# Performance work log

Measured on AMD Instinct MI355X. Metric: run time of the kernel, lower is better.

Reference implementation:

```python
import jax, jax.numpy as jnp
import numpy as np

N_NODES = 50000


def _sage_conv(x, src, dst, W_l, b_l, W_r):
    # PyG SAGEConv (aggr='mean'): out = lin_l(mean_{j in N(i)} x_j) + lin_r(x_i)
    # lin_l has bias, lin_r has no bias.
    neigh_sum = jax.ops.segment_sum(x[src], dst, num_segments=N_NODES)  # [N, F]
    deg = jax.ops.segment_sum(jnp.ones_like(dst, dtype=x.dtype), dst, num_segments=N_NODES)
    neigh_mean = neigh_sum / jnp.maximum(deg, 1.0)[:, None]
    return neigh_mean @ W_l.T + b_l + x @ W_r.T


def setup_inputs() -> dict:
    key = jax.random.key(0)
    ks = jax.random.split(key, 8)
    D, H, C = 768, 128, 4
    x = jax.random.normal(ks[0], (N_NODES, D), dtype=jnp.float32)
    edge_index = jax.random.randint(ks[1], (2, 800000), 0, N_NODES, dtype=jnp.int64)
    s1 = 1.0 / np.sqrt(D)
    s2 = 1.0 / np.sqrt(H)
    return {
        "x": x,
        "edge_index": edge_index,
        "W1_l": jax.random.uniform(ks[2], (H, D), jnp.float32, -s1, s1),
        "b1_l": jnp.zeros((H,), jnp.float32),
        "W1_r": jax.random.uniform(ks[3], (H, D), jnp.float32, -s1, s1),
        "W2_l": jax.random.uniform(ks[4], (C, H), jnp.float32, -s2, s2),
        "b2_l": jnp.zeros((C,), jnp.float32),
        "W2_r": jax.random.uniform(ks[5], (C, H), jnp.float32, -s2, s2),
    }


def reference(x, edge_index, W1_l, b1_l, W1_r, W2_l, b2_l, W2_r):
    src, dst = edge_index[0], edge_index[1]
    h = jax.nn.relu(_sage_conv(x, src, dst, W1_l, b1_l, W1_r))  # [N, H]
    out = _sage_conv(h, src, dst, W2_l, b2_l, W2_r)  # [N, C]
    return out
```

## Files before the change

kernel.cpp:

```cpp
#include <hip/hip_runtime.h>


typedef __bf16 bf16x8 __attribute__((ext_vector_type(8)));
typedef float  f32x4  __attribute__((ext_vector_type(4)));

__device__ __forceinline__ float bf16_lo(uint32_t w) {
    union { uint32_t u; float f; } c; c.u = w << 16; return c.f;
}
__device__ __forceinline__ float bf16_hi(uint32_t w) {
    union { uint32_t u; float f; } c; c.u = w & 0xffff0000u; return c.f;
}

__global__ __launch_bounds__(256)
void prep(const float* __restrict__ W1l, const float* __restrict__ W1r,
          __bf16* __restrict__ Wb, int* __restrict__ deg, int N)
{
    int i = blockIdx.x * 256 + threadIdx.x;
    if (i < N) deg[i] = 0;
    if (i < 256 * 768) {
        int n = i / 768, k = i - n * 768;
        float v = (n < 128) ? W1l[n * 768 + k] : W1r[(n - 128) * 768 + k];
        Wb[i] = (__bf16)v;
    }
}

__global__ __launch_bounds__(256)
void csr_count(const int* __restrict__ ei, int* __restrict__ deg, int E)
{
    int e = blockIdx.x * 256 + threadIdx.x;
    if (e >= E) return;
    atomicAdd(&deg[ei[E + e]], 1);
}

__global__ __launch_bounds__(1024)
void scan1(const int* __restrict__ deg, int* __restrict__ row_ptr,
           int* __restrict__ partials, int N)
{
    __shared__ int buf[1024];
    int i = blockIdx.x * 1024 + threadIdx.x;
    int v = (i < N) ? deg[i] : 0;
    int val = v;
    buf[threadIdx.x] = val;
    __syncthreads();
    for (int off = 1; off < 1024; off <<= 1) {
        int t = (threadIdx.x >= (unsigned)off) ? buf[threadIdx.x - off] : 0;
        __syncthreads();
        val += t;
        buf[threadIdx.x] = val;
        __syncthreads();
    }
    if (i < N) row_ptr[i] = val - v;
    if (threadIdx.x == 1023) partials[blockIdx.x] = val;
}

__global__ __launch_bounds__(1024)
void scan23(int* __restrict__ row_ptr, int* __restrict__ cursor,
            const int* __restrict__ partials, int N, int E, int nb)
{
    __shared__ int soff;
    int b = blockIdx.x;
    if (threadIdx.x < 64) {
        int lane = threadIdx.x;
        int v = (lane < nb) ? partials[lane] : 0;
        int s = v;
        #pragma unroll
        for (int off = 1; off < 64; off <<= 1) {
            int t = __shfl_up(s, off);
            if (lane >= off) s += t;
        }
        if (lane == b) soff = s - v;
    }
    __syncthreads();
    int off = soff;
    int i = b * 1024 + threadIdx.x;
    if (i < N) {
        int v = row_ptr[i] + off;
        row_ptr[i] = v;
        cursor[i]  = v;
    }
    if (b == 0 && threadIdx.x == 0) row_ptr[N] = E;
}

__global__ __launch_bounds__(256)
void gemm_fill(const float* __restrict__ A, const __bf16* __restrict__ Bw,
               __bf16* __restrict__ Cb, int M, int gblocks,
               const int* __restrict__ ei, int* __restrict__ cursor,
               int* __restrict__ csr_src, int E)
{
    constexpr int LDK = 72;
    __shared__ __bf16 As[64][LDK];
    __shared__ __bf16 Bs[64][LDK];
    const int tid = threadIdx.x;

    if ((int)blockIdx.x >= gblocks) {
        int e = (blockIdx.x - gblocks) * 256 + tid;
        if (e < E) {
            int src = ei[e];
            int dst = ei[E + e];
            int pos = atomicAdd(&cursor[dst], 1);
            csr_src[pos] = src;
        }
        return;
    }

    const int p   = blockIdx.x;
    const int xcd = p & 7, kk = p >> 3;
    const int q   = gblocks >> 3, rem = gblocks & 7;
    const int base = (xcd < rem) ? xcd * (q + 1) : rem * (q + 1) + (xcd - rem) * q;
    const int job = base + kk;
    const int bm  = (job >> 2) * 64;
    const int bn  = (job & 3) * 64;

    const int lane = tid & 63;
    const int wave = tid >> 6;
    const int wr = wave >> 1, wc = wave & 1;
    const int l15 = lane & 15;
    const int lk  = lane >> 4;

    f32x4 acc[2][2] = {};
    float4 apref[2][2];
    bf16x8 bpref[2];

    auto load_tile = [&](int k0) {
        #pragma unroll
        for (int it = 0; it < 2; ++it) {
            int v = it * 256 + tid;
            int row = v >> 3, kc = (v & 7) << 3;
            if (bm + row < M) {
                const float* src = A + (size_t)(bm + row) * 768 + k0 + kc;
                apref[it][0] = *(const float4*)src;
                apref[it][1] = *(const float4*)(src + 4);
            } else {
                apref[it][0] = make_float4(0.f, 0.f, 0.f, 0.f);
                apref[it][1] = make_float4(0.f, 0.f, 0.f, 0.f);
            }
            bpref[it] = *(const bf16x8*)(Bw + (size_t)(bn + row) * 768 + k0 + kc);
        }
    };

    load_tile(0);
    for (int kt = 0; kt < 12; ++kt) {
        if (kt) __syncthreads();
        #pragma unroll
        for (int it = 0; it < 2; ++it) {
            int v = it * 256 + tid;
            int row = v >> 3, kc = (v & 7) << 3;
            float4 f0 = apref[it][0], f1 = apref[it][1];
            bf16x8 b;
            b[0] = (__bf16)f0.x; b[1] = (__bf16)f0.y;
            b[2] = (__bf16)f0.z; b[3] = (__bf16)f0.w;
            b[4] = (__bf16)f1.x; b[5] = (__bf16)f1.y;
            b[6] = (__bf16)f1.z; b[7] = (__bf16)f1.w;
            *(bf16x8*)&As[row][kc] = b;
            *(bf16x8*)&Bs[row][kc] = bpref[it];
        }
        __syncthreads();
        if (kt < 11) load_tile((kt + 1) * 64);

        #pragma unroll
        for (int ks = 0; ks < 2; ++ks) {
            int koff = ks * 32 + lk * 8;
            bf16x8 af[2], bfr[2];
            #pragma unroll
            for (int i = 0; i < 2; ++i)
                af[i] = *(const bf16x8*)&As[wr * 32 + i * 16 + l15][koff];
            #pragma unroll
            for (int j = 0; j < 2; ++j)
                bfr[j] = *(const bf16x8*)&Bs[wc * 32 + j * 16 + l15][koff];
            #pragma unroll
            for (int i = 0; i < 2; ++i)
                #pragma unroll
                for (int j = 0; j < 2; ++j)
                    acc[i][j] = __builtin_amdgcn_mfma_f32_16x16x32_bf16(
                        af[i], bfr[j], acc[i][j], 0, 0, 0);
        }
    }

    __syncthreads();
    #pragma unroll
    for (int i = 0; i < 2; ++i)
        #pragma unroll
        for (int j = 0; j < 2; ++j)
            #pragma unroll
            for (int v = 0; v < 4; ++v)
                As[wr * 32 + i * 16 + lk * 4 + v][wc * 32 + j * 16 + l15] =
                    (__bf16)acc[i][j][v];
    __syncthreads();
    #pragma unroll
    for (int it = 0; it < 2; ++it) {
        int idx = it * 256 + tid;
        int row = idx >> 3, ch = idx & 7;
        if (bm + row < M)
            *(bf16x8*)(Cb + (size_t)(bm + row) * 256 + bn + ch * 8) =
                *(const bf16x8*)&As[row][ch * 8];
    }
}

__global__ __launch_bounds__(256)
void sage1_fused(const int* __restrict__ row_ptr, const int* __restrict__ csr_src,
                 const __bf16* __restrict__ pq, const float* __restrict__ b1,
                 const float* __restrict__ W2l, const float* __restrict__ W2r,
                 float* __restrict__ r, float* __restrict__ s, int N)
{
    __shared__ float Wl[512], Wr[512];
    for (int i = threadIdx.x; i < 512; i += 256) {
        Wl[i] = W2l[i];
        Wr[i] = W2r[i];
    }
    __syncthreads();

    int wid  = threadIdx.x >> 6;
    int lane = threadIdx.x & 63;
    int g = lane >> 3;
    int l = lane & 7;
    int n = blockIdx.x * 4 + wid;
    if (n >= N) return;
    int beg = row_ptr[n], end = row_ptr[n + 1];

    float a0[8] = {}, a1[8] = {};
    for (int eb = beg; eb < end; eb += 64) {
        int cnt = min(64, end - eb);
        int id = (eb + lane < end) ? csr_src[eb + lane] : 0;
        for (int t = 0; t < cnt; t += 8) {
            int src = __shfl(id, t + g);
            if (t + g < cnt) {
                const __bf16* row = pq + (size_t)src * 256;
                uint4 w0 = *(const uint4*)(row + l * 8);
                uint4 w1 = *(const uint4*)(row + 64 + l * 8);
                a0[0] += bf16_lo(w0.x); a0[1] += bf16_hi(w0.x);
                a0[2] += bf16_lo(w0.y); a0[3] += bf16_hi(w0.y);
                a0[4] += bf16_lo(w0.z); a0[5] += bf16_hi(w0.z);
                a0[6] += bf16_lo(w0.w); a0[7] += bf16_hi(w0.w);
                a1[0] += bf16_lo(w1.x); a1[1] += bf16_hi(w1.x);
                a1[2] += bf16_lo(w1.y); a1[3] += bf16_hi(w1.y);
                a1[4] += bf16_lo(w1.z); a1[5] += bf16_hi(w1.z);
                a1[6] += bf16_lo(w1.w); a1[7] += bf16_hi(w1.w);
            }
        }
    }
    #pragma unroll
    for (int c = 0; c < 8; ++c) {
        a0[c] += __shfl_xor(a0[c], 8);  a1[c] += __shfl_xor(a1[c], 8);
        a0[c] += __shfl_xor(a0[c], 16); a1[c] += __shfl_xor(a1[c], 16);
        a0[c] += __shfl_xor(a0[c], 32); a1[c] += __shfl_xor(a1[c], 32);
    }

    float inv = 1.0f / fmaxf((float)(end - beg), 1.0f);
    const __bf16* qrow = pq + (size_t)n * 256 + 128;
    uint4  qw0 = *(const uint4*)(qrow + l * 8);
    uint4  qw1 = *(const uint4*)(qrow + 64 + l * 8);
    float4 bv00 = *(const float4*)(b1 + l * 8);
    float4 bv01 = *(const float4*)(b1 + l * 8 + 4);
    float4 bv10 = *(const float4*)(b1 + 64 + l * 8);
    float4 bv11 = *(const float4*)(b1 + 64 + l * 8 + 4);
    float h0[8], h1[8];
    h0[0] = fmaxf(a0[0] * inv + bv00.x + bf16_lo(qw0.x), 0.f);
    h0[1] = fmaxf(a0[1] * inv + bv00.y + bf16_hi(qw0.x), 0.f);
    h0[2] = fmaxf(a0[2] * inv + bv00.z + bf16_lo(qw0.y), 0.f);
    h0[3] = fmaxf(a0[3] * inv + bv00.w + bf16_hi(qw0.y), 0.f);
    h0[4] = fmaxf(a0[4] * inv + bv01.x + bf16_lo(qw0.z), 0.f);
    h0[5] = fmaxf(a0[5] * inv + bv01.y + bf16_hi(qw0.z), 0.f);
    h0[6] = fmaxf(a0[6] * inv + bv01.z + bf16_lo(qw0.w), 0.f);
    h0[7] = fmaxf(a0[7] * inv + bv01.w + bf16_hi(qw0.w), 0.f);
    h1[0] = fmaxf(a1[0] * inv + bv10.x + bf16_lo(qw1.x), 0.f);
    h1[1] = fmaxf(a1[1] * inv + bv10.y + bf16_hi(qw1.x), 0.f);
    h1[2] = fmaxf(a1[2] * inv + bv10.z + bf16_lo(qw1.y), 0.f);
    h1[3] = fmaxf(a1[3] * inv + bv10.w + bf16_hi(qw1.y), 0.f);
    h1[4] = fmaxf(a1[4] * inv + bv11.x + bf16_lo(qw1.z), 0.f);
    h1[5] = fmaxf(a1[5] * inv + bv11.y + bf16_hi(qw1.z), 0.f);
    h1[6] = fmaxf(a1[6] * inv + bv11.z + bf16_lo(qw1.w), 0.f);
    h1[7] = fmaxf(a1[7] * inv + bv11.w + bf16_hi(qw1.w), 0.f);

    float part[8];
    #pragma unroll
    for (int c = 0; c < 4; ++c) {
        float pl = 0.f, pr = 0.f;
        #pragma unroll
        for (int j = 0; j < 8; ++j) {
            pl = fmaf(h0[j], Wl[c * 128 + l * 8 + j], pl);
            pl = fmaf(h1[j], Wl[c * 128 + 64 + l * 8 + j], pl);
            pr = fmaf(h0[j], Wr[c * 128 + l * 8 + j], pr);
            pr = fmaf(h1[j], Wr[c * 128 + 64 + l * 8 + j], pr);
        }
        part[c] = pl; part[4 + c] = pr;
    }
    #pragma unroll
    for (int off = 4; off; off >>= 1)
        #pragma unroll
        for (int c = 0; c < 8; ++c)
            part[c] += __shfl_xor(part[c], off);
    if (lane == 0) {
        *(float4*)(r + (size_t)n * 4) = make_float4(part[0], part[1], part[2], part[3]);
        *(float4*)(s + (size_t)n * 4) = make_float4(part[4], part[5], part[6], part[7]);
    }
}

__global__ __launch_bounds__(256)
void sage2_gather(const int* __restrict__ row_ptr, const int* __restrict__ csr_src,
                  const float* __restrict__ r, const float* __restrict__ s,
                  const float* __restrict__ b2, float* __restrict__ out, int N)
{
    int t = blockIdx.x * 256 + threadIdx.x;
    if (t >= N * 4) return;
    int n = t >> 2, c = t & 3;
    int beg = row_ptr[n], end = row_ptr[n + 1];
    float acc = 0.f;
    for (int e = beg; e < end; ++e)
        acc += r[(size_t)csr_src[e] * 4 + c];
    out[t] = acc / fmaxf((float)(end - beg), 1.0f) + b2[c] + s[t];
}

extern "C" void kernel_launch(void* const* d_in, const int* in_sizes, int n_in,
                              void* d_out, int out_size, void* d_ws, size_t ws_size,
                              hipStream_t stream)
{
    const float* x   = (const float*)d_in[0];
    const int*   ei  = (const int*)d_in[1];
    const float* W1l = (const float*)d_in[2];
    const float* b1l = (const float*)d_in[3];
    const float* W1r = (const float*)d_in[4];
    const float* W2l = (const float*)d_in[5];
    const float* b2l = (const float*)d_in[6];
    const float* W2r = (const float*)d_in[7];
    float* out = (float*)d_out;

    const int N = in_sizes[0] / 768;
    const int E = in_sizes[1] / 2;
    const int NB = (N + 1023) / 1024;
    const int mtiles  = (N + 63) / 64;
    const int gblocks = mtiles * 4;
    const int fblocks = (E + 255) / 256;

    char* ws = (char*)d_ws;
    size_t off = 0;
    auto alloc = [&](size_t bytes) -> void* {
        void* pp = ws + off;
        off += (bytes + 255) & ~(size_t)255;
        return pp;
    };
    __bf16* pq      = (__bf16*)alloc((size_t)N * 256 * 2);
    float*  r       = (float*)alloc((size_t)N * 4 * 4);
    float*  s       = (float*)alloc((size_t)N * 4 * 4);
    __bf16* Wb      = (__bf16*)alloc((size_t)256 * 768 * 2);
    int*    deg     = (int*)alloc((size_t)N * 4);
    int*    row_ptr = (int*)alloc((size_t)(N + 1) * 4);
    int*    cursor  = (int*)alloc((size_t)N * 4);
    int*    csr_src = (int*)alloc((size_t)E * 4);
    int*    partials= (int*)alloc((size_t)64 * 4);

    prep<<<(256 * 768 + 255) / 256, 256, 0, stream>>>(W1l, W1r, Wb, deg, N);

    csr_count<<<(E + 255) / 256, 256, 0, stream>>>(ei, deg, E);
    scan1<<<NB, 1024, 0, stream>>>(deg, row_ptr, partials, N);
    scan23<<<NB, 1024, 0, stream>>>(row_ptr, cursor, partials, N, E, NB);

    gemm_fill<<<gblocks + fblocks, 256, 0, stream>>>(x, Wb, pq, N, gblocks,
                                                     ei, cursor, csr_src, E);

    sage1_fused<<<(N + 3) / 4, 256, 0, stream>>>(row_ptr, csr_src, pq, b1l,
                                                 W2l, W2r, r, s, N);

    sage2_gather<<<(N * 4 + 255) / 256, 256, 0, stream>>>(row_ptr, csr_src, r, s, b2l, out, N);
}
```

Before: 203.5 us.

## Record per-edge slot in count pass and stagger GEMM K-loop start per block

The degree-count kernel now saves the value returned by its atomic as a per-edge slot. The CSR fill writes to row_ptr[dst]+slot[e] directly, so the second pass of atomics on a cursor array and the cursor initialization are gone. In exchange, an extra E-sized int array is written and then read back. Separately, each GEMM block starts its K-loop at a different rotated offset, so that blocks reading the same A rows or weight columns hit different K chunks at the same time and contend less.

```diff
diff --git a/kernel.cpp b/kernel.cpp
--- a/kernel.cpp
+++ b/kernel.cpp
@@ -25,11 +25,12 @@
 }
 
 __global__ __launch_bounds__(256)
-void csr_count(const int* __restrict__ ei, int* __restrict__ deg, int E)
+void csr_count(const int* __restrict__ ei, int* __restrict__ deg,
+               int* __restrict__ slot, int E)
 {
     int e = blockIdx.x * 256 + threadIdx.x;
     if (e >= E) return;
-    atomicAdd(&deg[ei[E + e]], 1);
+    slot[e] = atomicAdd(&deg[ei[E + e]], 1);
 }
 
 __global__ __launch_bounds__(1024)
@@ -54,8 +55,8 @@
 }
 
 __global__ __launch_bounds__(1024)
-void scan23(int* __restrict__ row_ptr, int* __restrict__ cursor,
-            const int* __restrict__ partials, int N, int E, int nb)
+void scan23(int* __restrict__ row_ptr, const int* __restrict__ partials,
+            int N, int E, int nb)
 {
     __shared__ int soff;
     int b = blockIdx.x;
@@ -73,19 +74,15 @@
     __syncthreads();
     int off = soff;
     int i = b * 1024 + threadIdx.x;
-    if (i < N) {
-        int v = row_ptr[i] + off;
-        row_ptr[i] = v;
-        cursor[i]  = v;
-    }
+    if (i < N) row_ptr[i] += off;
     if (b == 0 && threadIdx.x == 0) row_ptr[N] = E;
 }
 
 __global__ __launch_bounds__(256)
 void gemm_fill(const float* __restrict__ A, const __bf16* __restrict__ Bw,
                __bf16* __restrict__ Cb, int M, int gblocks,
-               const int* __restrict__ ei, int* __restrict__ cursor,
-               int* __restrict__ csr_src, int E)
+               const int* __restrict__ ei, const int* __restrict__ row_ptr,
+               const int* __restrict__ slot, int* __restrict__ csr_src, int E)
 {
     constexpr int LDK = 72;
     __shared__ __bf16 As[64][LDK];
@@ -97,8 +94,7 @@
         if (e < E) {
             int src = ei[e];
             int dst = ei[E + e];
-            int pos = atomicAdd(&cursor[dst], 1);
-            csr_src[pos] = src;
+            csr_src[row_ptr[dst] + slot[e]] = src;
         }
         return;
     }
@@ -110,6 +106,7 @@
     const int job = base + kk;
     const int bm  = (job >> 2) * 64;
     const int bn  = (job & 3) * 64;
+    const int k0off = job % 12;
 
     const int lane = tid & 63;
     const int wave = tid >> 6;
@@ -138,9 +135,11 @@
         }
     };
 
-    load_tile(0);
-    for (int kt = 0; kt < 12; ++kt) {
-        if (kt) __syncthreads();
+    load_tile(k0off * 64);
+    for (int t = 0; t < 12; ++t) {
+        const int kt  = (k0off + t) % 12;
+        const int ktn = (k0off + t + 1) % 12;
+        if (t) __syncthreads();
         #pragma unroll
         for (int it = 0; it < 2; ++it) {
             int v = it * 256 + tid;
@@ -155,7 +154,7 @@
             *(bf16x8*)&Bs[row][kc] = bpref[it];
         }
         __syncthreads();
-        if (kt < 11) load_tile((kt + 1) * 64);
+        if (t < 11) load_tile(ktn * 64);
 
         #pragma unroll
         for (int ks = 0; ks < 2; ++ks) {
@@ -344,18 +343,19 @@
     __bf16* Wb      = (__bf16*)alloc((size_t)256 * 768 * 2);
     int*    deg     = (int*)alloc((size_t)N * 4);
     int*    row_ptr = (int*)alloc((size_t)(N + 1) * 4);
-    int*    cursor  = (int*)alloc((size_t)N * 4);
+    int*    slot    = (int*)alloc((size_t)E * 4);
     int*    csr_src = (int*)alloc((size_t)E * 4);
     int*    partials= (int*)alloc((size_t)64 * 4);
 
     prep<<<(256 * 768 + 255) / 256, 256, 0, stream>>>(W1l, W1r, Wb, deg, N);
 
-    csr_count<<<(E + 255) / 256, 256, 0, stream>>>(ei, deg, E);
+    csr_count<<<(E + 255) / 256, 256, 0, stream>>>(ei, deg, slot, E);
     scan1<<<NB, 1024, 0, stream>>>(deg, row_ptr, partials, N);
-    scan23<<<NB, 1024, 0, stream>>>(row_ptr, cursor, partials, N, E, NB);
+    scan23<<<NB, 1024, 0, stream>>>(row_ptr, partials, N, E, NB);
 
     gemm_fill<<<gblocks + fblocks, 256, 0, stream>>>(x, Wb, pq, N, gblocks,
-                                                     ei, cursor, csr_src, E);
+                                                     ei, row_ptr, slot,
+                                                     csr_src, E);
 
     sage1_fused<<<(N + 3) / 4, 256, 0, stream>>>(row_ptr, csr_src, pq, b1l,
                                                  W2l, W2r, r, s, N);
```

Result: faster. 182.9 us (-10.1%).
